# Kernel tuning notes

Hardware: AMD Instinct MI355X
Metric: run time of the kernel (lower is better)

Reference implementation:

```python
import jax, jax.numpy as jnp
import numpy as np

H = 16       # num_attention_heads
HKV = 4      # num_key_value_heads
G = H // HKV # num_kv_groups
D = 128      # head_dim
ROT = 64     # rotary dim = head_dim * rope_partial_rotary_factor (0.5)
BLK = 64     # sparse_block_size
LOCAL = 8    # sparse_local_num_blocks
GLOB = 1     # sparse_global_num_blocks
SCALE = 1.0 / float(np.sqrt(D))
NEG = -1000000000.0


def _rotate_half(x):
    x1, x2 = x[..., : x.shape[-1] // 2], x[..., x.shape[-1] // 2 :]
    return jnp.concatenate((-x2, x1), axis=-1)


def _sparse_tables(n_blocks):
    """Static numpy tables mirroring _get_sparse_tables + causal masking.
    Returns idx (n,S) int32 gather table and mask (n, BLK, S, BLK) bool (True = masked)."""
    S = LOCAL + GLOB
    idx = np.zeros((n_blocks, S), np.int32)
    valid = np.zeros((n_blocks, S), bool)
    for i in range(n_blocks):
        sel = [g for g in range(GLOB) if g < n_blocks]
        sel += list(range(max(0, i - (LOCAL - 1)), i + 1))
        li = list(dict.fromkeys(sel))  # dedupe, keep order
        idx[i, : len(li)] = li
        valid[i, : len(li)] = True
    ii = np.arange(n_blocks)[:, None]
    dead = (~valid) | (idx > ii)          # invalid slot or future block
    selfb = idx == ii                     # diagonal block -> intra-causal
    jq = np.arange(BLK)[:, None]
    jk = np.arange(BLK)[None, :]
    intra = jk > jq                       # (q, k) strictly-upper masked
    mask = dead[:, None, :, None] | (selfb[:, None, :, None] & intra[None, :, None, :])
    return idx, mask                      # (n,S), (n,BLK,S,BLK)


def setup_inputs() -> dict:
    key = jax.random.key(0)
    ks = jax.random.split(key, 6)
    B_, T, HID = 2, 4096, 2048
    hidden_states = jax.random.normal(ks[0], (B_, T, HID), dtype=jnp.float32)
    # real RoPE tables for the rotary sub-dim
    inv_freq = 1.0 / (10000.0 ** (np.arange(0, ROT, 2, dtype=np.float32) / ROT))
    freqs = np.arange(T, dtype=np.float32)[:, None] * inv_freq[None, :]
    emb = np.concatenate([freqs, freqs], axis=-1)  # (T, ROT)
    cos = jnp.broadcast_to(jnp.asarray(np.cos(emb)), (B_, T, ROT))
    sin = jnp.broadcast_to(jnp.asarray(np.sin(emb)), (B_, T, ROT))
    Wq = jax.random.normal(ks[1], (H * D, HID), dtype=jnp.float32) * 0.02
    Wk = jax.random.normal(ks[2], (HKV * D, HID), dtype=jnp.float32) * 0.02
    Wv = jax.random.normal(ks[3], (HKV * D, HID), dtype=jnp.float32) * 0.02
    Wo = jax.random.normal(ks[4], (HID, H * D), dtype=jnp.float32) * 0.02
    return {"hidden_states": hidden_states, "cos": cos, "sin": sin,
            "Wq": Wq, "Wk": Wk, "Wv": Wv, "Wo": Wo}


def reference(hidden_states, cos, sin, Wq, Wk, Wv, Wo):
    B_, T, _ = hidden_states.shape
    q = (hidden_states @ Wq.T).reshape(B_, T, H, D).transpose(0, 2, 1, 3)    # (b,H,T,D)
    k = (hidden_states @ Wk.T).reshape(B_, T, HKV, D).transpose(0, 2, 1, 3)  # (b,HKV,T,D)
    v = (hidden_states @ Wv.T).reshape(B_, T, HKV, D).transpose(0, 2, 1, 3)
    # partial RoPE on first ROT dims
    c = cos[:, None, :, :]
    s = sin[:, None, :, :]
    def rope(x):
        xr, xp = x[..., :ROT], x[..., ROT:]
        xr = xr * c + _rotate_half(xr) * s
        return jnp.concatenate([xr, xp], axis=-1)
    q, k = rope(q), rope(k)
    # block-sparse local+global attention (prefill, T multiple of BLK)
    n = T // BLK
    idx_np, mask_np = _sparse_tables(n)
    idx = jnp.asarray(idx_np)
    mask = jnp.asarray(mask_np)  # (n, BLKq, S, BLKk)
    qb = q.reshape(B_, HKV, G, n, BLK, D)
    kb = k.reshape(B_, HKV, n, BLK, D)
    vb = v.reshape(B_, HKV, n, BLK, D)
    ksel = kb[:, :, idx]  # (b,HKV,n,S,BLK,D)
    vsel = vb[:, :, idx]
    scores = jnp.einsum('bhgnqd,bhnskd->bhgnqsk',
                        qb.astype(jnp.float32), ksel.astype(jnp.float32)) * SCALE
    scores = jnp.where(mask[None, None, None], NEG, scores)
    sh = scores.shape
    probs = jax.nn.softmax(scores.reshape(*sh[:5], -1), axis=-1).reshape(sh)
    out = jnp.einsum('bhgnqsk,bhnskd->bhgnqd', probs, vsel.astype(jnp.float32))
    out = out.astype(hidden_states.dtype).reshape(B_, H, T, D)
    out = out.transpose(0, 2, 1, 3).reshape(B_, T, H * D)
    return out @ Wo.T
```

## Files before the change

### kernel.cpp

```cpp
#include <hip/hip_runtime.h>
#include <hip/hip_bf16.h>

#define Hq   16
#define HKV  4
#define Dh   128
#define ROT  64
#define BLKQ 64
#define NBLK 64
#define Tlen 4096
#define Bsz  2
#define HID  2048
#define QKVC 3072
#define SCALE_C 0.08838834764831845f

typedef __attribute__((ext_vector_type(8))) short bf16x8;
typedef __attribute__((ext_vector_type(4))) float f32x4;

#define MFMA16(a, b, c) __builtin_amdgcn_mfma_f32_16x16x32_bf16((a), (b), (c), 0, 0, 0)

__device__ __forceinline__ void async_copy16(__hip_bfloat16* lds, const __hip_bfloat16* g) {
    __builtin_amdgcn_global_load_lds(
        (const __attribute__((address_space(1))) void*)g,
        (__attribute__((address_space(3))) void*)lds,
        16, 0, 0);
}

__global__ __launch_bounds__(256) void cvt_kernel(
    const float* __restrict__ s0, const float* __restrict__ s1,
    const float* __restrict__ s2, const float* __restrict__ s3,
    const float* __restrict__ s4,
    __hip_bfloat16* __restrict__ base,
    int n0, int n1, int n2, int n3, int n4)
{
    const float* src;
    size_t off, n;
    switch (blockIdx.y) {
        case 0:  src = s0; off = 0;                          n = n0; break;
        case 1:  src = s1; off = (size_t)n0;                 n = n1; break;
        case 2:  src = s2; off = (size_t)n0 + n1;            n = n2; break;
        case 3:  src = s3; off = (size_t)n0 + n1 + n2;       n = n3; break;
        default: src = s4; off = (size_t)n0 + n1 + n2 + n3;  n = n4; break;
    }
    __hip_bfloat16* dst = base + off;
    const size_t stride = (size_t)gridDim.x * 2048;
    for (size_t i = ((size_t)blockIdx.x * 256 + threadIdx.x) * 8; i < n; i += stride) {
        const float4 a = *(const float4*)(src + i);
        const float4 b = *(const float4*)(src + i + 4);
        union { bf16x8 v; __hip_bfloat16 e[8]; } u;
        u.e[0] = __float2bfloat16(a.x); u.e[1] = __float2bfloat16(a.y);
        u.e[2] = __float2bfloat16(a.z); u.e[3] = __float2bfloat16(a.w);
        u.e[4] = __float2bfloat16(b.x); u.e[5] = __float2bfloat16(b.y);
        u.e[6] = __float2bfloat16(b.z); u.e[7] = __float2bfloat16(b.w);
        *(bf16x8*)(dst + i) = u.v;
    }
}

template <bool ROPE_, bool F32OUT>
__global__ __launch_bounds__(256, 2) void gemm128db(
    const __hip_bfloat16* __restrict__ A,
    const __hip_bfloat16* __restrict__ B0,
    const __hip_bfloat16* __restrict__ B1,
    const __hip_bfloat16* __restrict__ B2,
    int n1c, int n2c,
    void* __restrict__ C,
    int M, int N, int K,
    const float* __restrict__ cosb,
    const float* __restrict__ sinb)
{
    __shared__ __align__(16) __hip_bfloat16 As[2][128 * 64];
    __shared__ __align__(16) __hip_bfloat16 Bs[2][128 * 64];

    const int m0 = blockIdx.y * 128;
    const int n0 = blockIdx.x * 128;
    const __hip_bfloat16* Bp;
    int nb;
    if (n0 < n1c)      { Bp = B0; nb = n0; }
    else if (n0 < n2c) { Bp = B1; nb = n0 - n1c; }
    else               { Bp = B2; nb = n0 - n2c; }

    const int tid  = threadIdx.x;
    const int lane = tid & 63;
    const int w    = tid >> 6;
    const int wm   = (w >> 1) * 64;
    const int wn   = (w & 1) * 64;
    const int lr   = lane >> 3;
    const int lc   = lane & 7;
    const int m16  = lane & 15;
    const int q8   = lane >> 4;
    const int NT   = K >> 6;

    f32x4 acc[4][4] = {};

    auto stageA = [&](int buf, int kc) {
        #pragma unroll
        for (int ii = 0; ii < 4; ++ii) {
            const int r8 = w * 32 + ii * 8;
            const int r  = r8 + lr;
            const int cg = lc ^ (r & 7);
            async_copy16(&As[buf][r8 * 64], A + (size_t)(m0 + r) * K + kc + cg * 8);
        }
    };
    auto stageB = [&](int buf, int kc) {
        #pragma unroll
        for (int ii = 0; ii < 4; ++ii) {
            const int r8 = w * 32 + ii * 8;
            const int r  = r8 + lr;
            const int cg = lc ^ (r & 7);
            async_copy16(&Bs[buf][r8 * 64], Bp + (size_t)(nb + r) * K + kc + cg * 8);
        }
    };

    stageA(0, 0);
    stageB(0, 0);
    asm volatile("s_waitcnt vmcnt(0)" ::: "memory");
    __builtin_amdgcn_s_barrier();

    for (int u = 0; u < NT; ++u) {
        const int P  = u & 1;
        const int kN = (u + 1 < NT ? u + 1 : 0) << 6;
        const __hip_bfloat16* Ap_ = As[P];
        const __hip_bfloat16* Bq_ = Bs[P];

        bf16x8 a0[4], b0[4], a1[4], b1[4];

        #pragma unroll
        for (int t = 0; t < 4; ++t) {
            const int row = wm + t * 16 + m16;
            const int csA = q8 ^ (row & 7);
            a0[t] = *(const bf16x8*)&Ap_[row * 64 + csA * 8];
            const int col = wn + t * 16 + m16;
            const int csB = q8 ^ (col & 7);
            b0[t] = *(const bf16x8*)&Bq_[col * 64 + csB * 8];
        }
        stageA(P ^ 1, kN);
        asm volatile("s_waitcnt lgkmcnt(0)" ::: "memory");
        __builtin_amdgcn_s_setprio(1);
        #pragma unroll
        for (int i = 0; i < 4; ++i)
            #pragma unroll
            for (int j = 0; j < 4; ++j)
                acc[i][j] = MFMA16(a0[i], b0[j], acc[i][j]);
        __builtin_amdgcn_s_setprio(0);

        #pragma unroll
        for (int t = 0; t < 4; ++t) {
            const int row = wm + t * 16 + m16;
            const int csA = (4 + q8) ^ (row & 7);
            a1[t] = *(const bf16x8*)&Ap_[row * 64 + csA * 8];
            const int col = wn + t * 16 + m16;
            const int csB = (4 + q8) ^ (col & 7);
            b1[t] = *(const bf16x8*)&Bq_[col * 64 + csB * 8];
        }
        stageB(P ^ 1, kN);
        asm volatile("s_waitcnt lgkmcnt(0)" ::: "memory");
        __builtin_amdgcn_s_setprio(1);
        #pragma unroll
        for (int i = 0; i < 4; ++i)
            #pragma unroll
            for (int j = 0; j < 4; ++j)
                acc[i][j] = MFMA16(a1[i], b1[j], acc[i][j]);
        __builtin_amdgcn_s_setprio(0);

        asm volatile("s_waitcnt vmcnt(0)" ::: "memory");
        __builtin_amdgcn_s_barrier();
    }

    if (ROPE_ && n0 < n2c && wn == 0) {
        #pragma unroll
        for (int i = 0; i < 4; ++i)
            #pragma unroll
            for (int r = 0; r < 4; ++r) {
                const int bt = m0 + wm + i * 16 + q8 * 4 + r;
                #pragma unroll
                for (int j = 0; j < 2; ++j) {
                    const int d = j * 16 + m16;
                    const float c = cosb[(size_t)bt * ROT + d];
                    const float s = sinb[(size_t)bt * ROT + d];
                    const float x1 = acc[i][j][r];
                    const float x2 = acc[i][j + 2][r];
                    acc[i][j][r]     = x1 * c - x2 * s;
                    acc[i][j + 2][r] = x2 * c + x1 * s;
                }
            }
    }

    #pragma unroll
    for (int i = 0; i < 4; ++i)
        #pragma unroll
        for (int j = 0; j < 4; ++j)
            #pragma unroll
            for (int r = 0; r < 4; ++r) {
                const int row = m0 + wm + i * 16 + q8 * 4 + r;
                const int col = n0 + wn + j * 16 + m16;
                if (F32OUT)
                    ((float*)C)[(size_t)row * N + col] = acc[i][j][r];
                else
                    ((__hip_bfloat16*)C)[(size_t)row * N + col] =
                        __float2bfloat16(acc[i][j][r]);
            }
}

__global__ __launch_bounds__(256) void vtrans_kernel(
    const __hip_bfloat16* __restrict__ qkv,
    __hip_bfloat16* __restrict__ vtg)
{
    const int tb = blockIdx.x;
    const int pr = blockIdx.y;
    const __hip_bfloat16* src =
        qkv + ((size_t)(pr >> 2) * Tlen + tb * 64) * QKVC + HID + 512 + (pr & 3) * Dh;
    __hip_bfloat16* dst = vtg + (size_t)pr * Dh * Tlen + tb * 64;
    const int tid = threadIdx.x;
    #pragma unroll
    for (int t2 = 0; t2 < 4; ++t2) {
        const int c  = tid + t2 * 256;
        const int d  = c >> 3;
        const int t0 = (c & 7) * 8;
        union { bf16x8 v; __hip_bfloat16 e[8]; } u;
        #pragma unroll
        for (int j = 0; j < 8; ++j)
            u.e[j] = src[(size_t)(t0 + j) * QKVC + d];
        *(bf16x8*)(dst + (size_t)d * Tlen + t0) = u.v;
    }
}

__global__ __launch_bounds__(256, 3) void attn_kernel(
    const __hip_bfloat16* __restrict__ qkv,
    const __hip_bfloat16* __restrict__ vtg,
    __hip_bfloat16* __restrict__ outb)
{
    const int i   = blockIdx.x;
    const int h   = blockIdx.y;
    const int b   = blockIdx.z;
    const int kvh = h >> 2;
    const int tid  = threadIdx.x;
    const int lane = tid & 63;
    const int w    = tid >> 6;
    const int m16  = lane & 15;
    const int q8   = lane >> 4;

    __shared__ __align__(16) __hip_bfloat16 Ks[64 * 136];
    __shared__ __align__(16) __hip_bfloat16 VT[128 * 72];
    __shared__ __align__(16) __hip_bfloat16 Pb[4][16 * 72];

    bf16x8 qf[4];
    {
        const __hip_bfloat16* qp =
            qkv + (size_t)(b * Tlen + i * BLKQ + w * 16 + m16) * QKVC + h * Dh + q8 * 8;
        for (int ks = 0; ks < 4; ++ks) qf[ks] = *(const bf16x8*)(qp + ks * 32);
    }

    f32x4 o[8] = {};
    float mrow[4] = {-1e30f, -1e30f, -1e30f, -1e30f};
    float lrow[4] = {0.f, 0.f, 0.f, 0.f};

    const int nsel = (i + 1 < 9) ? (i + 1) : 9;
    auto kb_of = [&](int j) { return (i <= 7) ? j : ((j == 0) ? 0 : (i - 8 + j)); };

    const __hip_bfloat16* vtbase = vtg + (size_t)(b * HKV + kvh) * Dh * Tlen;

    bf16x8 kr[4], vr[4];
    {
        const int kb0 = kb_of(0);
        const __hip_bfloat16* kbase =
            qkv + (size_t)(b * Tlen + kb0 * BLKQ) * QKVC + HID + kvh * Dh;
        #pragma unroll
        for (int t = 0; t < 4; ++t) {
            const int c = tid + t * 256;
            kr[t] = *(const bf16x8*)(kbase + (size_t)(c >> 4) * QKVC + (c & 15) * 8);
            vr[t] = *(const bf16x8*)(vtbase + (size_t)(c >> 3) * Tlen
                                     + kb0 * BLKQ + (c & 7) * 8);
        }
    }

    for (int j = 0; j < nsel; ++j) {
        const int kb = kb_of(j);

        __syncthreads();
        #pragma unroll
        for (int t = 0; t < 4; ++t) {
            const int c = tid + t * 256;
            *(bf16x8*)&Ks[(c >> 4) * 136 + (c & 15) * 8] = kr[t];
        }
        #pragma unroll
        for (int t = 0; t < 4; ++t) {
            const int c = tid + t * 256;
            *(bf16x8*)&VT[(c >> 3) * 72 + (c & 7) * 8] = vr[t];
        }
        __syncthreads();

        if (j + 1 < nsel) {
            const int kbn = kb_of(j + 1);
            const __hip_bfloat16* kbase =
                qkv + (size_t)(b * Tlen + kbn * BLKQ) * QKVC + HID + kvh * Dh;
            #pragma unroll
            for (int t = 0; t < 4; ++t) {
                const int c = tid + t * 256;
                kr[t] = *(const bf16x8*)(kbase + (size_t)(c >> 4) * QKVC + (c & 15) * 8);
                vr[t] = *(const bf16x8*)(vtbase + (size_t)(c >> 3) * Tlen
                                         + kbn * BLKQ + (c & 7) * 8);
            }
        }

        float sv[4][4];
        __builtin_amdgcn_s_setprio(1);
        for (int nt = 0; nt < 4; ++nt) {
            f32x4 s = {0.f, 0.f, 0.f, 0.f};
            for (int ks = 0; ks < 4; ++ks) {
                bf16x8 kf = *(const bf16x8*)&Ks[(nt * 16 + m16) * 136 + ks * 32 + q8 * 8];
                s = MFMA16(qf[ks], kf, s);
            }
            for (int r = 0; r < 4; ++r) sv[nt][r] = s[r] * SCALE_C;
        }
        __builtin_amdgcn_s_setprio(0);
        if (kb == i) {
            for (int nt = 0; nt < 4; ++nt) {
                const int key = nt * 16 + m16;
                for (int r = 0; r < 4; ++r) {
                    const int qr = w * 16 + q8 * 4 + r;
                    if (key > qr) sv[nt][r] = -1e9f;
                }
            }
        }

        float alpha[4];
        for (int r = 0; r < 4; ++r) {
            float mx = fmaxf(fmaxf(sv[0][r], sv[1][r]), fmaxf(sv[2][r], sv[3][r]));
            for (int off = 1; off < 16; off <<= 1) mx = fmaxf(mx, __shfl_xor(mx, off, 64));
            const float newm = fmaxf(mrow[r], mx);
            alpha[r] = __expf(mrow[r] - newm);
            mrow[r] = newm;
            float rs = 0.f;
            for (int nt = 0; nt < 4; ++nt) {
                const float p = __expf(sv[nt][r] - newm);
                sv[nt][r] = p;
                rs += p;
            }
            for (int off = 1; off < 16; off <<= 1) rs += __shfl_xor(rs, off, 64);
            lrow[r] = lrow[r] * alpha[r] + rs;
        }

        __hip_bfloat16* Pw = &Pb[w][0];
        for (int nt = 0; nt < 4; ++nt)
            for (int r = 0; r < 4; ++r)
                Pw[(q8 * 4 + r) * 72 + nt * 16 + m16] = __float2bfloat16(sv[nt][r]);

        for (int dt = 0; dt < 8; ++dt)
            for (int r = 0; r < 4; ++r)
                o[dt][r] *= alpha[r];

        asm volatile("s_waitcnt lgkmcnt(0)" ::: "memory");
        __builtin_amdgcn_sched_barrier(0);

        __builtin_amdgcn_s_setprio(1);
        for (int kk = 0; kk < 2; ++kk) {
            bf16x8 pf = *(const bf16x8*)&Pw[m16 * 72 + kk * 32 + q8 * 8];
            for (int dt = 0; dt < 8; ++dt) {
                bf16x8 vf = *(const bf16x8*)&VT[(dt * 16 + m16) * 72 + kk * 32 + q8 * 8];
                o[dt] = MFMA16(pf, vf, o[dt]);
            }
        }
        __builtin_amdgcn_s_setprio(0);
    }

    float rcp[4];
    for (int r = 0; r < 4; ++r) rcp[r] = 1.0f / lrow[r];
    __hip_bfloat16* op = outb + (size_t)(b * Tlen + i * BLKQ) * (Hq * Dh) + h * Dh;
    for (int dt = 0; dt < 8; ++dt)
        for (int r = 0; r < 4; ++r) {
            const float val = o[dt][r] * rcp[r];
            op[(size_t)(w * 16 + q8 * 4 + r) * (Hq * Dh) + dt * 16 + m16] =
                __float2bfloat16(val);
        }
}

extern "C" void kernel_launch(void* const* d_in, const int* in_sizes, int n_in,
                              void* d_out, int out_size, void* d_ws, size_t ws_size,
                              hipStream_t stream) {
    const float* hs   = (const float*)d_in[0];
    const float* cosb = (const float*)d_in[1];
    const float* sinb = (const float*)d_in[2];
    const float* Wq   = (const float*)d_in[3];
    const float* Wk   = (const float*)d_in[4];
    const float* Wv   = (const float*)d_in[5];
    const float* Wo   = (const float*)d_in[6];

    const int M = Bsz * Tlen;
    const int nHS = M * HID;
    const int nWq = Hq * Dh * HID;
    const int nWk = HKV * Dh * HID;
    const int nWv = nWk;
    const int nWo = HID * Hq * Dh;

    __hip_bfloat16* hsb  = (__hip_bfloat16*)d_ws;
    __hip_bfloat16* wqb  = hsb + nHS;
    __hip_bfloat16* wkb  = wqb + nWq;
    __hip_bfloat16* wvb  = wkb + nWk;
    __hip_bfloat16* wob  = wvb + nWv;
    __hip_bfloat16* qkv  = wob + nWo;
    __hip_bfloat16* attn = qkv + (size_t)M * QKVC;
    __hip_bfloat16* vtg  = attn + (size_t)M * (Hq * Dh);

    cvt_kernel<<<dim3(8192, 5), 256, 0, stream>>>(
        hs, Wq, Wk, Wv, Wo, hsb, nHS, nWq, nWk, nWv, nWo);
    gemm128db<true, false><<<dim3(QKVC / 128, M / 128), 256, 0, stream>>>(
        hsb, wqb, wkb, wvb, HID, HID + 512, qkv, M, QKVC, HID, cosb, sinb);
    vtrans_kernel<<<dim3(NBLK, Bsz * HKV), 256, 0, stream>>>(qkv, vtg);
    attn_kernel<<<dim3(NBLK, Hq, Bsz), 256, 0, stream>>>(qkv, vtg, attn);
    gemm128db<false, true><<<dim3(HID / 128, M / 128), 256, 0, stream>>>(
        attn, wob, wob, wob, HID, HID, d_out, M, HID, HID, nullptr, nullptr);
}
```

Baseline: 430.1 us.

## Deepen GEMM global-to-LDS prefetch to two tiles ahead with partial vmcnt waits

The GEMM main loop now prefetches k-tiles two iterations ahead instead of one. It loads all A/B fragments from LDS up front, barriers, then reissues async copies into the just-consumed buffer. It waits only for the older tile via vmcnt(8) rather than draining all outstanding loads, so memory latency overlaps with more MFMA work. The cost is an extra barrier per iteration and more register pressure from holding all fragments at once.

```diff
diff --git a/kernel.cpp b/kernel.cpp
--- a/kernel.cpp
+++ b/kernel.cpp
@@ -112,48 +112,42 @@
 
     stageA(0, 0);
     stageB(0, 0);
-    asm volatile("s_waitcnt vmcnt(0)" ::: "memory");
+    stageA(1, 64);
+    stageB(1, 64);
+    asm volatile("s_waitcnt vmcnt(8)" ::: "memory");
     __builtin_amdgcn_s_barrier();
 
     for (int u = 0; u < NT; ++u) {
         const int P  = u & 1;
-        const int kN = (u + 1 < NT ? u + 1 : 0) << 6;
         const __hip_bfloat16* Ap_ = As[P];
         const __hip_bfloat16* Bq_ = Bs[P];
 
         bf16x8 a0[4], b0[4], a1[4], b1[4];
-
         #pragma unroll
         for (int t = 0; t < 4; ++t) {
             const int row = wm + t * 16 + m16;
-            const int csA = q8 ^ (row & 7);
-            a0[t] = *(const bf16x8*)&Ap_[row * 64 + csA * 8];
             const int col = wn + t * 16 + m16;
-            const int csB = q8 ^ (col & 7);
-            b0[t] = *(const bf16x8*)&Bq_[col * 64 + csB * 8];
-        }
-        stageA(P ^ 1, kN);
+            a0[t] = *(const bf16x8*)&Ap_[row * 64 + ((q8)     ^ (row & 7)) * 8];
+            b0[t] = *(const bf16x8*)&Bq_[col * 64 + ((q8)     ^ (col & 7)) * 8];
+            a1[t] = *(const bf16x8*)&Ap_[row * 64 + ((4 + q8) ^ (row & 7)) * 8];
+            b1[t] = *(const bf16x8*)&Bq_[col * 64 + ((4 + q8) ^ (col & 7)) * 8];
+        }
         asm volatile("s_waitcnt lgkmcnt(0)" ::: "memory");
+        __builtin_amdgcn_sched_barrier(0);
+        __builtin_amdgcn_s_barrier();
+        __builtin_amdgcn_sched_barrier(0);
+
+        if (u + 2 < NT) {
+            stageA(P, (u + 2) << 6);
+            stageB(P, (u + 2) << 6);
+        }
+
         __builtin_amdgcn_s_setprio(1);
         #pragma unroll
         for (int i = 0; i < 4; ++i)
             #pragma unroll
             for (int j = 0; j < 4; ++j)
                 acc[i][j] = MFMA16(a0[i], b0[j], acc[i][j]);
-        __builtin_amdgcn_s_setprio(0);
-
-        #pragma unroll
-        for (int t = 0; t < 4; ++t) {
-            const int row = wm + t * 16 + m16;
-            const int csA = (4 + q8) ^ (row & 7);
-            a1[t] = *(const bf16x8*)&Ap_[row * 64 + csA * 8];
-            const int col = wn + t * 16 + m16;
-            const int csB = (4 + q8) ^ (col & 7);
-            b1[t] = *(const bf16x8*)&Bq_[col * 64 + csB * 8];
-        }
-        stageB(P ^ 1, kN);
-        asm volatile("s_waitcnt lgkmcnt(0)" ::: "memory");
-        __builtin_amdgcn_s_setprio(1);
         #pragma unroll
         for (int i = 0; i < 4; ++i)
             #pragma unroll
@@ -161,7 +155,11 @@
                 acc[i][j] = MFMA16(a1[i], b1[j], acc[i][j]);
         __builtin_amdgcn_s_setprio(0);
 
-        asm volatile("s_waitcnt vmcnt(0)" ::: "memory");
+        if (u + 2 < NT) {
+            asm volatile("s_waitcnt vmcnt(8)" ::: "memory");
+        } else {
+            asm volatile("s_waitcnt vmcnt(0)" ::: "memory");
+        }
         __builtin_amdgcn_s_barrier();
     }
 
```

Measured after the change: 415.8 us. 3.3% less time.
